# Kernel optimization log

Hardware: AMD Instinct MI355X
Metric: run time of the kernel (lower is better)

The kernel has to match this reference:

```python
import jax, jax.numpy as jnp
import numpy as np

N_CELL, N_WELL = 200000, 2000
E_CC, E_CW = 1200000, 200000
CF, WF, H = 16, 8, 128
NUM_PHASES, OUT_SEQ = 3, 25
OUT = NUM_PHASES * OUT_SEQ  # 75


def setup_inputs() -> dict:
    key = jax.random.key(0)
    ks = jax.random.split(key, 24)
    p = lambda k, shp: jax.random.normal(k, shp, dtype=jnp.float32) * 0.02
    return {
        "cell_x": jax.random.normal(ks[0], (N_CELL, CF), dtype=jnp.float32),
        "well_x": jax.random.normal(ks[1], (N_WELL, WF), dtype=jnp.float32),
        "edge_index_cell": jax.random.randint(ks[2], (2, E_CC), 0, N_CELL),
        "edge_well_src": jax.random.randint(ks[3], (E_CW,), 0, N_CELL),
        "edge_well_dst": jax.random.randint(ks[4], (E_CW,), 0, N_WELL),
        # input projections
        "W_cell": p(ks[5], (CF, H)), "b_cell": jnp.zeros((H,), jnp.float32),
        "W_well": p(ks[6], (WF, H)), "b_well": jnp.zeros((H,), jnp.float32),
        # SAGEConv cell->cell: lin_l (on aggregated neighbors, has bias), lin_r (on root, no bias)
        "Wl_cc": p(ks[7], (H, H)), "bl_cc": jnp.zeros((H,), jnp.float32),
        "Wr_cc": p(ks[8], (H, H)),
        # SAGEConv cell->well (bipartite)
        "Wl_cw": p(ks[9], (H, H)), "bl_cw": jnp.zeros((H,), jnp.float32),
        "Wr_cw": p(ks[10], (H, H)),
        # well MLP
        "W_m1": p(ks[11], (H, H)), "b_m1": jnp.zeros((H,), jnp.float32),
        "W_m2": p(ks[12], (H, OUT)), "b_m2": jnp.zeros((OUT,), jnp.float32),
    }


def _mean_aggr(msgs, dst, num_segments):
    # PyG 'mean' aggregation: sum per destination / neighbor count; 0 for isolated nodes.
    s = jax.ops.segment_sum(msgs, dst, num_segments=num_segments)
    c = jax.ops.segment_sum(jnp.ones((dst.shape[0], 1), msgs.dtype), dst, num_segments=num_segments)
    return s / jnp.maximum(c, 1.0)


def reference(cell_x, well_x, edge_index_cell, edge_well_src, edge_well_dst,
              W_cell, b_cell, W_well, b_well,
              Wl_cc, bl_cc, Wr_cc, Wl_cw, bl_cw, Wr_cw,
              W_m1, b_m1, W_m2, b_m2):
    cell_h = cell_x @ W_cell + b_cell                      # [N_cell, H]
    well_h = well_x @ W_well + b_well                      # [N_well, H]

    # SAGEConv(cell_h, edge_index_cell): gather source feats, mean-scatter to dst
    src, dst = edge_index_cell[0], edge_index_cell[1]
    agg_c = _mean_aggr(cell_h[src], dst, N_CELL)           # [N_cell, H]
    cell_h = agg_c @ Wl_cc + bl_cc + cell_h @ Wr_cc

    # Bipartite SAGEConv((cell_h, well_h), edge_well): aggregate cells into wells
    agg_w = _mean_aggr(cell_h[edge_well_src], edge_well_dst, N_WELL)  # [N_well, H]
    well_h = agg_w @ Wl_cw + bl_cw + well_h @ Wr_cw

    # well MLP head
    h = jax.nn.relu(well_h @ W_m1 + b_m1)
    out = h @ W_m2 + b_m2                                  # [N_well, 75]
    return out.reshape(-1, NUM_PHASES, OUT_SEQ)            # [N_well, 3, 25]
```

## Files before the change

kernel.cpp:

```cpp
#include <hip/hip_runtime.h>

#define N_CELL 200000
#define N_WELL 2000
#define E_CC   1200000
#define E_CW   200000
#define CF     16
#define WF     8
#define H      128
#define OUTF   75

#define CAP_C  16
#define CAP_W  224
#define OVF_CAP 16384
#define WPB    4

__device__ __forceinline__ float b2f(unsigned short u) {
    union { unsigned int i; float f; } v; v.i = ((unsigned int)u) << 16; return v.f;
}
__device__ __forceinline__ unsigned short f2b(float f) {
    union { float f; unsigned int i; } v; v.f = f;
    unsigned int i = v.i;
    return (unsigned short)((i + 0x7fffu + ((i >> 16) & 1u)) >> 16);
}
__device__ __forceinline__ float lo16(unsigned int v) { return b2f((unsigned short)(v & 0xffffu)); }
__device__ __forceinline__ float hi16(unsigned int v) { return b2f((unsigned short)(v >> 16)); }
__device__ __forceinline__ float ldf(const void* p, int i, int bf) {
    return bf ? b2f(((const unsigned short*)p)[i]) : ((const float*)p)[i];
}

__global__ __launch_bounds__(256) void k_sniff(const unsigned int* __restrict__ x, int* __restrict__ flag)
{
    __shared__ int cnt[256];
    int t = threadIdx.x;
    unsigned int d = x[t];
    unsigned int e = (d >> 7) & 0xffu;
    cnt[t] = (e >= 110u && e <= 135u) ? 1 : 0;
    __syncthreads();
    for (int o = 128; o > 0; o >>= 1) { if (t < o) cnt[t] += cnt[t + o]; __syncthreads(); }
    if (t == 0) flag[0] = (cnt[0] >= 192) ? 1 : 0;
}

__global__ __launch_bounds__(128) void k_precomp(const void* __restrict__ W_cell,
                                                 const void* __restrict__ b_cell,
                                                 const void* __restrict__ Wl,
                                                 const void* __restrict__ Wr,
                                                 const void* __restrict__ bl,
                                                 const int* __restrict__ flag,
                                                 float* __restrict__ G1, float* __restrict__ G2,
                                                 float* __restrict__ g1v, float* __restrict__ g2v)
{
    int f = threadIdx.x, b = blockIdx.x, bf = flag[0];
    if (b < 16) {
        float s1 = 0.f, s2 = 0.f;
        for (int j = 0; j < H; ++j) {
            float wc = ldf(W_cell, b * H + j, bf);
            s1 += wc * ldf(Wl, j * H + f, bf);
            s2 += wc * ldf(Wr, j * H + f, bf);
        }
        G1[b * H + f] = s1; G2[b * H + f] = s2;
    } else {
        float s1 = 0.f, s2 = 0.f;
        for (int j = 0; j < H; ++j) {
            float bc = ldf(b_cell, j, bf);
            s1 += bc * ldf(Wl, j * H + f, bf);
            s2 += bc * ldf(Wr, j * H + f, bf);
        }
        g1v[f] = s1; g2v[f] = s2 + ldf(bl, f, bf);
    }
}

__global__ __launch_bounds__(128) void k_precomp2(const float* __restrict__ G1, const float* __restrict__ G2,
                                                  const float* __restrict__ g1v, const float* __restrict__ g2v,
                                                  const void* __restrict__ Wl_cw,
                                                  const void* __restrict__ bl_cw,
                                                  const void* __restrict__ Wr_cw,
                                                  const void* __restrict__ W_well,
                                                  const void* __restrict__ b_well,
                                                  const int* __restrict__ flag,
                                                  float* __restrict__ A1, float* __restrict__ A2,
                                                  float* __restrict__ Bm,
                                                  float* __restrict__ a1, float* __restrict__ a2,
                                                  float* __restrict__ b0)
{
    int f = threadIdx.x, b = blockIdx.x, bf = flag[0];
    if (b < 16) {
        float s1 = 0.f, s2 = 0.f;
        for (int j = 0; j < H; ++j) {
            float wl = ldf(Wl_cw, j * H + f, bf);
            s1 += G1[b * H + j] * wl;
            s2 += G2[b * H + j] * wl;
        }
        A1[b * H + f] = s1; A2[b * H + f] = s2;
    } else if (b < 24) {
        int k = b - 16;
        float s = 0.f;
        for (int j = 0; j < H; ++j)
            s += ldf(W_well, k * H + j, bf) * ldf(Wr_cw, j * H + f, bf);
        Bm[k * H + f] = s;
    } else {
        float s1 = 0.f, s2 = 0.f, s3 = 0.f;
        for (int j = 0; j < H; ++j) {
            float wl = ldf(Wl_cw, j * H + f, bf);
            s1 += g1v[j] * wl;
            s2 += g2v[j] * wl;
            s3 += ldf(b_well, j, bf) * ldf(Wr_cw, j * H + f, bf);
        }
        a1[f] = s1; a2[f] = s2; b0[f] = s3 + ldf(bl_cw, f, bf);
    }
}

__global__ __launch_bounds__(256) void k_cvt(const void* __restrict__ Wm1, const void* __restrict__ Wm2,
                                             const void* __restrict__ bm1, const void* __restrict__ bm2,
                                             const int* __restrict__ flag,
                                             float* __restrict__ Wm1f, float* __restrict__ Wm2f,
                                             float* __restrict__ bm1f, float* __restrict__ bm2f)
{
    int i = blockIdx.x * 256 + threadIdx.x, bf = flag[0];
    if (i < H * H) Wm1f[i] = ldf(Wm1, i, bf);
    else if (i < H * H + H * OUTF) Wm2f[i - H * H] = ldf(Wm2, i - H * H, bf);
    else if (i < H * H + H * OUTF + H) bm1f[i - H * H - H * OUTF] = ldf(bm1, i - H * H - H * OUTF, bf);
    else if (i < H * H + H * OUTF + H + OUTF) bm2f[i - H * H - H * OUTF - H] = ldf(bm2, i - H * H - H * OUTF - H, bf);
}

__global__ void k_mark(const int* __restrict__ ews, unsigned char* __restrict__ mark)
{
    int i = blockIdx.x * 256 + threadIdx.x;
    if (i < E_CW) {
        unsigned c = (unsigned)ews[i];
        if (c < N_CELL) mark[c] = 1;
    }
}

__global__ void k_build(const int* __restrict__ cc_src, const int* __restrict__ cc_dst,
                        const int* __restrict__ ews, const int* __restrict__ ewd,
                        const unsigned char* __restrict__ mark,
                        int* __restrict__ counts_c, int* __restrict__ counts_w,
                        int* __restrict__ buckets_c, int* __restrict__ buckets_w,
                        int* __restrict__ ovf_cnt, int2* __restrict__ ovf)
{
    int i = blockIdx.x * 256 + threadIdx.x;
    if (i < E_CC) {
        unsigned d = (unsigned)cc_dst[i];
        if (d < N_CELL && mark[d]) {
            int s = atomicAdd(&counts_c[d], 1);
            if (s < CAP_C) buckets_c[d * CAP_C + s] = cc_src[i];
            else {
                int p = atomicAdd(ovf_cnt, 1);
                if (p < OVF_CAP) { ovf[p].x = (int)d; ovf[p].y = cc_src[i]; }
            }
        }
    } else if (i < E_CC + E_CW) {
        int j = i - E_CC;
        unsigned d = (unsigned)ewd[j];
        if (d < N_WELL) {
            int s = atomicAdd(&counts_w[d], 1);
            if (s < CAP_W) buckets_w[d * CAP_W + s] = ews[j];
        }
    }
}

__global__ __launch_bounds__(256) void k_aggA(const void* __restrict__ xr,
                                              const int* __restrict__ flag,
                                              const unsigned char* __restrict__ mark,
                                              const int* __restrict__ counts_c,
                                              const int* __restrict__ buckets_c,
                                              float* __restrict__ y)
{
    int gid = (blockIdx.x * 256 + threadIdx.x) >> 3;
    int jl = threadIdx.x & 7;
    if (gid >= N_CELL) return;
    if (!mark[gid]) return;
    int bf = flag[0];
    int cnt = counts_c[gid]; if (cnt < 0) cnt = 0;
    int lim = (cnt < CAP_C) ? cnt : CAP_C;
    float acc[16];
#pragma unroll
    for (int k = 0; k < 16; ++k) acc[k] = 0.f;

    for (int j = jl; j < lim; j += 8) {
        unsigned s = (unsigned)buckets_c[gid * CAP_C + j]; if (s >= N_CELL) s = 0;
        if (bf) {
            uint4 a = ((const uint4*)xr)[(size_t)s * 2];
            uint4 b = ((const uint4*)xr)[(size_t)s * 2 + 1];
            acc[0] += lo16(a.x);  acc[1] += hi16(a.x);
            acc[2] += lo16(a.y);  acc[3] += hi16(a.y);
            acc[4] += lo16(a.z);  acc[5] += hi16(a.z);
            acc[6] += lo16(a.w);  acc[7] += hi16(a.w);
            acc[8] += lo16(b.x);  acc[9] += hi16(b.x);
            acc[10] += lo16(b.y); acc[11] += hi16(b.y);
            acc[12] += lo16(b.z); acc[13] += hi16(b.z);
            acc[14] += lo16(b.w); acc[15] += hi16(b.w);
        } else {
            const float4* p = (const float4*)xr + (size_t)s * 4;
#pragma unroll
            for (int q = 0; q < 4; ++q) {
                float4 v = p[q];
                acc[4 * q]     += v.x; acc[4 * q + 1] += v.y;
                acc[4 * q + 2] += v.z; acc[4 * q + 3] += v.w;
            }
        }
    }
#pragma unroll
    for (int m = 1; m < 8; m <<= 1) {
#pragma unroll
        for (int k = 0; k < 16; ++k) acc[k] += __shfl_xor(acc[k], m, 64);
    }
    float sc = (cnt > 0) ? (1.0f / (float)cnt) : 0.0f;
    float2 st; st.x = acc[2 * jl] * sc; st.y = acc[2 * jl + 1] * sc;
    ((float2*)y)[(size_t)gid * 8 + jl] = st;
}

__global__ __launch_bounds__(256) void k_ovf(const void* __restrict__ xr,
                                             const int* __restrict__ flag,
                                             const int* __restrict__ ovf_cnt,
                                             const int2* __restrict__ ovf,
                                             const int* __restrict__ counts_c,
                                             float* __restrict__ y)
{
    int gid = (blockIdx.x * 256 + threadIdx.x) >> 3;
    int jl = threadIdx.x & 7;
    int n = ovf_cnt[0]; if (n > OVF_CAP) n = OVF_CAP;
    if (gid >= n) return;
    int bf = flag[0];
    unsigned d = (unsigned)ovf[gid].x; if (d >= N_CELL) d = 0;
    unsigned s = (unsigned)ovf[gid].y; if (s >= N_CELL) s = 0;
    int cnt = counts_c[d];
    float inv = (cnt > 0) ? (1.0f / (float)cnt) : 0.0f;
    float v0, v1;
    if (bf) {
        unsigned int u = ((const unsigned int*)xr)[(size_t)s * 8 + jl];
        v0 = lo16(u); v1 = hi16(u);
    } else {
        v0 = ((const float*)xr)[(size_t)s * 16 + 2 * jl];
        v1 = ((const float*)xr)[(size_t)s * 16 + 2 * jl + 1];
    }
    atomicAdd(&y[(size_t)d * 16 + 2 * jl], v0 * inv);
    atomicAdd(&y[(size_t)d * 16 + 2 * jl + 1], v1 * inv);
}

__global__ __launch_bounds__(256) void k_wellagg(const void* __restrict__ xr,
                                                 const int* __restrict__ flag,
                                                 const float* __restrict__ y,
                                                 const int* __restrict__ counts_c,
                                                 const int* __restrict__ counts_w,
                                                 const int* __restrict__ buckets_w,
                                                 const void* __restrict__ wx,
                                                 const float* __restrict__ A1, const float* __restrict__ A2,
                                                 const float* __restrict__ Bm,
                                                 const float* __restrict__ a1, const float* __restrict__ a2,
                                                 const float* __restrict__ b0,
                                                 float* __restrict__ Z)
{
    __shared__ float sP[16], sR[16], sq[1];
    int w = blockIdx.x, t = threadIdx.x, bf = flag[0];
    int g = t >> 3, jl = t & 7;
    if (t < 16) { sP[t] = 0.f; sR[t] = 0.f; }
    if (t == 16) sq[0] = 0.f;
    __syncthreads();

    int cntw = counts_w[w]; if (cntw < 0) cntw = 0;
    int lim = (cntw < CAP_W) ? cntw : CAP_W;

    float p0 = 0.f, p1 = 0.f, r0 = 0.f, r1 = 0.f, qn = 0.f;
    const unsigned int* x32 = (const unsigned int*)xr;
    const float* xf = (const float*)xr;

    for (int e = g; e < lim; e += 32) {
        unsigned c = (unsigned)buckets_w[w * CAP_W + e]; if (c >= N_CELL) c = 0;
        float2 yv = ((const float2*)y)[(size_t)c * 8 + jl];
        p0 += yv.x; p1 += yv.y;
        if (bf) {
            unsigned int u = x32[(size_t)c * 8 + jl];
            r0 += lo16(u); r1 += hi16(u);
        } else {
            r0 += xf[(size_t)c * 16 + 2 * jl];
            r1 += xf[(size_t)c * 16 + 2 * jl + 1];
        }
        if (jl == 0) qn += (counts_c[c] > 0) ? 1.0f : 0.0f;
    }
    atomicAdd(&sP[2 * jl], p0);
    atomicAdd(&sP[2 * jl + 1], p1);
    atomicAdd(&sR[2 * jl], r0);
    atomicAdd(&sR[2 * jl + 1], r1);
    if (jl == 0 && qn != 0.f) atomicAdd(&sq[0], qn);
    __syncthreads();

    int f = t;
    if (f < H) {
        float inv = (cntw > 0) ? (1.0f / (float)cntw) : 0.0f;
        float mask = (cntw > 0) ? 1.0f : 0.0f;
        float wh = (sq[0] * inv) * a1[f] + a2[f];
#pragma unroll
        for (int k = 0; k < 16; ++k)
            wh += (sP[k] * inv) * A1[k * H + f] + (sR[k] * inv) * A2[k * H + f];
        wh *= mask;
        wh += b0[f];
#pragma unroll
        for (int k = 0; k < WF; ++k)
            wh += ldf(wx, w * WF + k, bf) * Bm[k * H + f];
        Z[(size_t)w * H + f] = wh;
    }
}

__global__ __launch_bounds__(128) void k_head(const float* __restrict__ Z,
                                              const float* __restrict__ Wm1f, const float* __restrict__ Wm2f,
                                              const float* __restrict__ bm1f, const float* __restrict__ bm2f,
                                              const int* __restrict__ flag,
                                              void* __restrict__ outp)
{
    __shared__ float sz[WPB][H], sh[WPB][H];
    int w0 = blockIdx.x * WPB, t = threadIdx.x, bf = flag[0];
    float4 zv = ((const float4*)(Z + (size_t)w0 * H))[t];
    ((float4*)&sz[0][0])[t] = zv;
    __syncthreads();

    float acc[WPB];
#pragma unroll
    for (int i = 0; i < WPB; ++i) acc[i] = bm1f[t];
    for (int k = 0; k < H; ++k) {
        float wm = Wm1f[k * H + t];
#pragma unroll
        for (int i = 0; i < WPB; ++i) acc[i] += sz[i][k] * wm;
    }
#pragma unroll
    for (int i = 0; i < WPB; ++i) sh[i][t] = fmaxf(acc[i], 0.f);
    __syncthreads();

    if (t < OUTF) {
        float o[WPB];
#pragma unroll
        for (int i = 0; i < WPB; ++i) o[i] = bm2f[t];
        for (int k = 0; k < H; ++k) {
            float wm = Wm2f[k * OUTF + t];
#pragma unroll
            for (int i = 0; i < WPB; ++i) o[i] += sh[i][k] * wm;
        }
        if (bf) {
#pragma unroll
            for (int i = 0; i < WPB; ++i)
                ((unsigned short*)outp)[(size_t)(w0 + i) * OUTF + t] = f2b(o[i]);
        } else {
#pragma unroll
            for (int i = 0; i < WPB; ++i)
                ((float*)outp)[(size_t)(w0 + i) * OUTF + t] = o[i];
        }
    }
}

extern "C" void kernel_launch(void* const* d_in, const int* in_sizes, int n_in,
                              void* d_out, int out_size, void* d_ws, size_t ws_size,
                              hipStream_t stream)
{
    const void* cell_x = d_in[0];
    const void* well_x = d_in[1];
    const int* eic = (const int*)d_in[2];
    const int* ews = (const int*)d_in[3];
    const int* ewd = (const int*)d_in[4];
    const void* W_cell = d_in[5];
    const void* b_cell = d_in[6];
    const void* W_well = d_in[7];
    const void* b_well = d_in[8];
    const void* Wl_cc = d_in[9];
    const void* bl_cc = d_in[10];
    const void* Wr_cc = d_in[11];
    const void* Wl_cw = d_in[12];
    const void* bl_cw = d_in[13];
    const void* Wr_cw = d_in[14];
    const void* W_m1 = d_in[15];
    const void* b_m1 = d_in[16];
    const void* W_m2 = d_in[17];
    const void* b_m2 = d_in[18];
    (void)in_sizes; (void)n_in; (void)out_size; (void)ws_size;

    const int* cc_src = eic;
    const int* cc_dst = eic + E_CC;

    char* wsp = (char*)d_ws;
    size_t off = 0;
    auto carve = [&](size_t bytes) -> char* {
        char* p = wsp + off;
        off = (off + bytes + 255) & ~(size_t)255;
        return p;
    };

    float* G1   = (float*)carve(16 * H * 4);
    float* G2   = (float*)carve(16 * H * 4);
    float* g1v  = (float*)carve(H * 4);
    float* g2v  = (float*)carve(H * 4);
    float* A1   = (float*)carve(16 * H * 4);
    float* A2   = (float*)carve(16 * H * 4);
    float* Bm   = (float*)carve(WF * H * 4);
    float* a1   = (float*)carve(H * 4);
    float* a2   = (float*)carve(H * 4);
    float* b0   = (float*)carve(H * 4);
    float* Wm1f = (float*)carve(H * H * 4);
    float* Wm2f = (float*)carve(H * OUTF * 4);
    float* bm1f = (float*)carve(H * 4);
    float* bm2f = (float*)carve(OUTF * 4);
    int*   flag = (int*)carve(256);
    size_t zero_beg = off;
    int*   counts   = (int*)carve((size_t)(N_CELL + N_WELL) * 4);
    int*   counts_c = counts;
    int*   counts_w = counts + N_CELL;
    unsigned char* mark = (unsigned char*)carve((size_t)N_CELL);
    int*   ovf_cnt  = (int*)carve(256);
    size_t zero_end = off;
    int*   buckets_c = (int*)carve((size_t)N_CELL * CAP_C * 4);
    int*   buckets_w = (int*)carve((size_t)N_WELL * CAP_W * 4);
    float* y         = (float*)carve((size_t)N_CELL * 16 * 4);
    int2*  ovf       = (int2*)carve((size_t)OVF_CAP * 8);
    float* Z         = (float*)carve((size_t)N_WELL * H * 4);

    k_sniff<<<1, 256, 0, stream>>>((const unsigned int*)cell_x, flag);
    hipMemsetAsync((char*)d_ws + zero_beg, 0, zero_end - zero_beg, stream);
    k_precomp<<<17, 128, 0, stream>>>(W_cell, b_cell, Wl_cc, Wr_cc, bl_cc, flag, G1, G2, g1v, g2v);
    k_precomp2<<<25, 128, 0, stream>>>(G1, G2, g1v, g2v, Wl_cw, bl_cw, Wr_cw, W_well, b_well, flag,
                                       A1, A2, Bm, a1, a2, b0);
    k_cvt<<<(H * H + H * OUTF + H + OUTF + 255) / 256, 256, 0, stream>>>(W_m1, W_m2, b_m1, b_m2, flag,
                                                                         Wm1f, Wm2f, bm1f, bm2f);
    k_mark<<<(E_CW + 255) / 256, 256, 0, stream>>>(ews, mark);
    k_build<<<(E_CC + E_CW + 255) / 256, 256, 0, stream>>>(cc_src, cc_dst, ews, ewd, mark,
                                                           counts_c, counts_w, buckets_c, buckets_w,
                                                           ovf_cnt, ovf);
    k_aggA<<<(N_CELL * 8 + 255) / 256, 256, 0, stream>>>(cell_x, flag, mark, counts_c, buckets_c, y);
    k_ovf<<<(OVF_CAP * 8 + 255) / 256, 256, 0, stream>>>(cell_x, flag, ovf_cnt, ovf, counts_c, y);
    k_wellagg<<<N_WELL, 256, 0, stream>>>(cell_x, flag, y, counts_c, counts_w, buckets_w,
                                          well_x, A1, A2, Bm, a1, a2, b0, Z);
    k_head<<<N_WELL / WPB, 128, 0, stream>>>(Z, Wm1f, Wm2f, bm1f, bm2f, flag, d_out);
}
```

Baseline: 276.9 us.

## Replace per-cell edge buckets with bin-sorted edges and shared-memory aggregation

Cell-to-cell edges are no longer scattered into fixed-capacity per-destination buckets with an overflow path. They are now counting-sorted into 782 bins of 256 destination cells each, using a histogram, a scan and a scatter pass, and packed as source index plus local destination. Each bin is then aggregated in LDS with shared atomics, which also yields the neighbor counts. This removes the random global atomics on per-cell counters and the overflow kernel, but it reads the edge list twice and adds two kernel launches. The aggregation now relies on LDS float atomics.

```diff
diff --git a/kernel.cpp b/kernel.cpp
--- a/kernel.cpp
+++ b/kernel.cpp
@@ -9,10 +9,13 @@
 #define H      128
 #define OUTF   75
 
-#define CAP_C  16
 #define CAP_W  224
-#define OVF_CAP 16384
 #define WPB    4
+
+#define CPB    256
+#define NBIN   782
+#define NBLK_P 128
+#define CHUNK  9375
 
 __device__ __forceinline__ float b2f(unsigned short u) {
     union { unsigned int i; float f; } v; v.i = ((unsigned int)u) << 16; return v.f;
@@ -122,120 +125,147 @@
     else if (i < H * H + H * OUTF + H + OUTF) bm2f[i - H * H - H * OUTF - H] = ldf(bm2, i - H * H - H * OUTF - H, bf);
 }
 
-__global__ void k_mark(const int* __restrict__ ews, unsigned char* __restrict__ mark)
+__global__ void k_markw(const int* __restrict__ ews, const int* __restrict__ ewd,
+                        unsigned char* __restrict__ mark,
+                        int* __restrict__ counts_w, int* __restrict__ buckets_w)
 {
     int i = blockIdx.x * 256 + threadIdx.x;
     if (i < E_CW) {
         unsigned c = (unsigned)ews[i];
         if (c < N_CELL) mark[c] = 1;
-    }
-}
-
-__global__ void k_build(const int* __restrict__ cc_src, const int* __restrict__ cc_dst,
-                        const int* __restrict__ ews, const int* __restrict__ ewd,
-                        const unsigned char* __restrict__ mark,
-                        int* __restrict__ counts_c, int* __restrict__ counts_w,
-                        int* __restrict__ buckets_c, int* __restrict__ buckets_w,
-                        int* __restrict__ ovf_cnt, int2* __restrict__ ovf)
-{
-    int i = blockIdx.x * 256 + threadIdx.x;
-    if (i < E_CC) {
-        unsigned d = (unsigned)cc_dst[i];
-        if (d < N_CELL && mark[d]) {
-            int s = atomicAdd(&counts_c[d], 1);
-            if (s < CAP_C) buckets_c[d * CAP_C + s] = cc_src[i];
-            else {
-                int p = atomicAdd(ovf_cnt, 1);
-                if (p < OVF_CAP) { ovf[p].x = (int)d; ovf[p].y = cc_src[i]; }
-            }
-        }
-    } else if (i < E_CC + E_CW) {
-        int j = i - E_CC;
-        unsigned d = (unsigned)ewd[j];
+        unsigned d = (unsigned)ewd[i];
         if (d < N_WELL) {
             int s = atomicAdd(&counts_w[d], 1);
-            if (s < CAP_W) buckets_w[d * CAP_W + s] = ews[j];
-        }
-    }
-}
-
-__global__ __launch_bounds__(256) void k_aggA(const void* __restrict__ xr,
-                                              const int* __restrict__ flag,
+            if (s < CAP_W) buckets_w[d * CAP_W + s] = ews[i];
+        }
+    }
+}
+
+__global__ __launch_bounds__(256) void k_hist(const int* __restrict__ cc_dst,
                                               const unsigned char* __restrict__ mark,
-                                              const int* __restrict__ counts_c,
-                                              const int* __restrict__ buckets_c,
-                                              float* __restrict__ y)
-{
-    int gid = (blockIdx.x * 256 + threadIdx.x) >> 3;
-    int jl = threadIdx.x & 7;
-    if (gid >= N_CELL) return;
-    if (!mark[gid]) return;
-    int bf = flag[0];
-    int cnt = counts_c[gid]; if (cnt < 0) cnt = 0;
-    int lim = (cnt < CAP_C) ? cnt : CAP_C;
-    float acc[16];
-#pragma unroll
-    for (int k = 0; k < 16; ++k) acc[k] = 0.f;
-
-    for (int j = jl; j < lim; j += 8) {
-        unsigned s = (unsigned)buckets_c[gid * CAP_C + j]; if (s >= N_CELL) s = 0;
+                                              int* __restrict__ bin_cnt)
+{
+    __shared__ int hl[NBIN];
+    int t = threadIdx.x;
+    for (int i = t; i < NBIN; i += 256) hl[i] = 0;
+    __syncthreads();
+    int beg = blockIdx.x * CHUNK, end = beg + CHUNK; if (end > E_CC) end = E_CC;
+    for (int e = beg + t; e < end; e += 256) {
+        unsigned d = (unsigned)cc_dst[e];
+        if (d < N_CELL && mark[d]) atomicAdd(&hl[d >> 8], 1);
+    }
+    __syncthreads();
+    for (int i = t; i < NBIN; i += 256) if (hl[i]) atomicAdd(&bin_cnt[i], hl[i]);
+}
+
+__global__ __launch_bounds__(1024) void k_scanbins(const int* __restrict__ bin_cnt,
+                                                   int* __restrict__ bin_off, int* __restrict__ bin_cur)
+{
+    __shared__ int sm[1024];
+    int t = threadIdx.x;
+    sm[t] = (t < NBIN) ? bin_cnt[t] : 0;
+    __syncthreads();
+    for (int o = 1; o < 1024; o <<= 1) {
+        int u = (t >= o) ? sm[t - o] : 0;
+        __syncthreads();
+        sm[t] += u;
+        __syncthreads();
+    }
+    if (t < NBIN) {
+        int v = sm[t];
+        bin_off[t + 1] = v;
+        bin_cur[t] = v - bin_cnt[t];
+        if (t == 0) bin_off[0] = 0;
+    }
+}
+
+__global__ __launch_bounds__(256) void k_scatter(const int* __restrict__ cc_src,
+                                                 const int* __restrict__ cc_dst,
+                                                 const unsigned char* __restrict__ mark,
+                                                 int* __restrict__ bin_cur,
+                                                 unsigned int* __restrict__ binned)
+{
+    __shared__ int hl[NBIN];
+    __shared__ int cur[NBIN];
+    int t = threadIdx.x;
+    for (int i = t; i < NBIN; i += 256) hl[i] = 0;
+    __syncthreads();
+    int beg = blockIdx.x * CHUNK, end = beg + CHUNK; if (end > E_CC) end = E_CC;
+    for (int e = beg + t; e < end; e += 256) {
+        unsigned d = (unsigned)cc_dst[e];
+        if (d < N_CELL && mark[d]) atomicAdd(&hl[d >> 8], 1);
+    }
+    __syncthreads();
+    for (int i = t; i < NBIN; i += 256)
+        cur[i] = hl[i] ? atomicAdd(&bin_cur[i], hl[i]) : 0;
+    __syncthreads();
+    for (int e = beg + t; e < end; e += 256) {
+        unsigned d = (unsigned)cc_dst[e];
+        if (d < N_CELL && mark[d]) {
+            unsigned s = (unsigned)cc_src[e]; if (s >= N_CELL) s = 0;
+            int slot = atomicAdd(&cur[d >> 8], 1);
+            if ((unsigned)slot < E_CC)
+                binned[slot] = s | ((d & 255u) << 18);
+        }
+    }
+}
+
+__global__ __launch_bounds__(256) void k_binagg(const void* __restrict__ xr,
+                                                const int* __restrict__ flag,
+                                                const int* __restrict__ bin_off,
+                                                const unsigned int* __restrict__ binned,
+                                                float* __restrict__ y, int* __restrict__ counts_c)
+{
+    __shared__ float yl[CPB * 16];
+    __shared__ int   dl[CPB];
+    __shared__ float il[CPB];
+    int b = blockIdx.x, t = threadIdx.x, bf = flag[0];
+    for (int i = t; i < CPB * 16; i += 256) yl[i] = 0.f;
+    if (t < CPB) dl[t] = 0;
+    __syncthreads();
+    int beg = bin_off[b], end = bin_off[b + 1];
+    if (beg < 0) beg = 0;
+    if (end > E_CC) end = E_CC;
+    for (int e = beg + t; e < end; e += 256) {
+        unsigned p = binned[e];
+        unsigned s = p & 0x3FFFFu; if (s >= N_CELL) s = 0;
+        int dloc = (p >> 18) & 255;
+        atomicAdd(&dl[dloc], 1);
+        float* yr = &yl[dloc * 16];
         if (bf) {
             uint4 a = ((const uint4*)xr)[(size_t)s * 2];
-            uint4 b = ((const uint4*)xr)[(size_t)s * 2 + 1];
-            acc[0] += lo16(a.x);  acc[1] += hi16(a.x);
-            acc[2] += lo16(a.y);  acc[3] += hi16(a.y);
-            acc[4] += lo16(a.z);  acc[5] += hi16(a.z);
-            acc[6] += lo16(a.w);  acc[7] += hi16(a.w);
-            acc[8] += lo16(b.x);  acc[9] += hi16(b.x);
-            acc[10] += lo16(b.y); acc[11] += hi16(b.y);
-            acc[12] += lo16(b.z); acc[13] += hi16(b.z);
-            acc[14] += lo16(b.w); acc[15] += hi16(b.w);
+            uint4 bq = ((const uint4*)xr)[(size_t)s * 2 + 1];
+            atomicAdd(&yr[0],  lo16(a.x));  atomicAdd(&yr[1],  hi16(a.x));
+            atomicAdd(&yr[2],  lo16(a.y));  atomicAdd(&yr[3],  hi16(a.y));
+            atomicAdd(&yr[4],  lo16(a.z));  atomicAdd(&yr[5],  hi16(a.z));
+            atomicAdd(&yr[6],  lo16(a.w));  atomicAdd(&yr[7],  hi16(a.w));
+            atomicAdd(&yr[8],  lo16(bq.x)); atomicAdd(&yr[9],  hi16(bq.x));
+            atomicAdd(&yr[10], lo16(bq.y)); atomicAdd(&yr[11], hi16(bq.y));
+            atomicAdd(&yr[12], lo16(bq.z)); atomicAdd(&yr[13], hi16(bq.z));
+            atomicAdd(&yr[14], lo16(bq.w)); atomicAdd(&yr[15], hi16(bq.w));
         } else {
-            const float4* p = (const float4*)xr + (size_t)s * 4;
+            const float4* pp = (const float4*)xr + (size_t)s * 4;
 #pragma unroll
             for (int q = 0; q < 4; ++q) {
-                float4 v = p[q];
-                acc[4 * q]     += v.x; acc[4 * q + 1] += v.y;
-                acc[4 * q + 2] += v.z; acc[4 * q + 3] += v.w;
+                float4 v = pp[q];
+                atomicAdd(&yr[4 * q],     v.x); atomicAdd(&yr[4 * q + 1], v.y);
+                atomicAdd(&yr[4 * q + 2], v.z); atomicAdd(&yr[4 * q + 3], v.w);
             }
         }
     }
-#pragma unroll
-    for (int m = 1; m < 8; m <<= 1) {
-#pragma unroll
-        for (int k = 0; k < 16; ++k) acc[k] += __shfl_xor(acc[k], m, 64);
-    }
-    float sc = (cnt > 0) ? (1.0f / (float)cnt) : 0.0f;
-    float2 st; st.x = acc[2 * jl] * sc; st.y = acc[2 * jl + 1] * sc;
-    ((float2*)y)[(size_t)gid * 8 + jl] = st;
-}
-
-__global__ __launch_bounds__(256) void k_ovf(const void* __restrict__ xr,
-                                             const int* __restrict__ flag,
-                                             const int* __restrict__ ovf_cnt,
-                                             const int2* __restrict__ ovf,
-                                             const int* __restrict__ counts_c,
-                                             float* __restrict__ y)
-{
-    int gid = (blockIdx.x * 256 + threadIdx.x) >> 3;
-    int jl = threadIdx.x & 7;
-    int n = ovf_cnt[0]; if (n > OVF_CAP) n = OVF_CAP;
-    if (gid >= n) return;
-    int bf = flag[0];
-    unsigned d = (unsigned)ovf[gid].x; if (d >= N_CELL) d = 0;
-    unsigned s = (unsigned)ovf[gid].y; if (s >= N_CELL) s = 0;
-    int cnt = counts_c[d];
-    float inv = (cnt > 0) ? (1.0f / (float)cnt) : 0.0f;
-    float v0, v1;
-    if (bf) {
-        unsigned int u = ((const unsigned int*)xr)[(size_t)s * 8 + jl];
-        v0 = lo16(u); v1 = hi16(u);
-    } else {
-        v0 = ((const float*)xr)[(size_t)s * 16 + 2 * jl];
-        v1 = ((const float*)xr)[(size_t)s * 16 + 2 * jl + 1];
-    }
-    atomicAdd(&y[(size_t)d * 16 + 2 * jl], v0 * inv);
-    atomicAdd(&y[(size_t)d * 16 + 2 * jl + 1], v1 * inv);
+    __syncthreads();
+    if (t < CPB) {
+        int d = dl[t];
+        il[t] = (d > 0) ? (1.0f / (float)d) : 0.f;
+        int c = b * CPB + t;
+        if (c < N_CELL) counts_c[c] = d;
+    }
+    __syncthreads();
+    size_t base = (size_t)b * CPB * 16;
+    for (int i = t; i < CPB * 16; i += 256) {
+        int cl = i >> 4;
+        if (b * CPB + cl < N_CELL) y[base + i] = yl[i] * il[cl];
+    }
 }
 
 __global__ __launch_bounds__(256) void k_wellagg(const void* __restrict__ xr,
@@ -403,12 +433,13 @@
     int*   counts_c = counts;
     int*   counts_w = counts + N_CELL;
     unsigned char* mark = (unsigned char*)carve((size_t)N_CELL);
-    int*   ovf_cnt  = (int*)carve(256);
+    int*   bin_cnt = (int*)carve((size_t)(NBIN + 2) * 4);
     size_t zero_end = off;
-    int*   buckets_c = (int*)carve((size_t)N_CELL * CAP_C * 4);
+    int*   bin_off  = (int*)carve((size_t)(NBIN + 2) * 4);
+    int*   bin_cur  = (int*)carve((size_t)(NBIN + 2) * 4);
+    unsigned int* binned = (unsigned int*)carve((size_t)E_CC * 4);
     int*   buckets_w = (int*)carve((size_t)N_WELL * CAP_W * 4);
-    float* y         = (float*)carve((size_t)N_CELL * 16 * 4);
-    int2*  ovf       = (int2*)carve((size_t)OVF_CAP * 8);
+    float* y         = (float*)carve((size_t)NBIN * CPB * 16 * 4);
     float* Z         = (float*)carve((size_t)N_WELL * H * 4);
 
     k_sniff<<<1, 256, 0, stream>>>((const unsigned int*)cell_x, flag);
@@ -418,12 +449,11 @@
                                        A1, A2, Bm, a1, a2, b0);
     k_cvt<<<(H * H + H * OUTF + H + OUTF + 255) / 256, 256, 0, stream>>>(W_m1, W_m2, b_m1, b_m2, flag,
                                                                          Wm1f, Wm2f, bm1f, bm2f);
-    k_mark<<<(E_CW + 255) / 256, 256, 0, stream>>>(ews, mark);
-    k_build<<<(E_CC + E_CW + 255) / 256, 256, 0, stream>>>(cc_src, cc_dst, ews, ewd, mark,
-                                                           counts_c, counts_w, buckets_c, buckets_w,
-                                                           ovf_cnt, ovf);
-    k_aggA<<<(N_CELL * 8 + 255) / 256, 256, 0, stream>>>(cell_x, flag, mark, counts_c, buckets_c, y);
-    k_ovf<<<(OVF_CAP * 8 + 255) / 256, 256, 0, stream>>>(cell_x, flag, ovf_cnt, ovf, counts_c, y);
+    k_markw<<<(E_CW + 255) / 256, 256, 0, stream>>>(ews, ewd, mark, counts_w, buckets_w);
+    k_hist<<<NBLK_P, 256, 0, stream>>>(cc_dst, mark, bin_cnt);
+    k_scanbins<<<1, 1024, 0, stream>>>(bin_cnt, bin_off, bin_cur);
+    k_scatter<<<NBLK_P, 256, 0, stream>>>(cc_src, cc_dst, mark, bin_cur, binned);
+    k_binagg<<<NBIN, 256, 0, stream>>>(cell_x, flag, bin_off, binned, y, counts_c);
     k_wellagg<<<N_WELL, 256, 0, stream>>>(cell_x, flag, y, counts_c, counts_w, buckets_w,
                                           well_x, A1, A2, Bm, a1, a2, b0, Z);
     k_head<<<N_WELL / WPB, 128, 0, stream>>>(Z, Wm1f, Wm2f, bm1f, bm2f, flag, d_out);
```

Measured after the change: 367.6 us. 1.33x slower.

## Fold weight conversion into precompute, merge well bucketing with marking, batch edge loads

Applied to the files above, without the earlier changes.

Merges the k_cvt weight conversion into k_precomp2 through extra blocks and fuses well-edge bucketing into the marking kernel, which removes two launches. k_build now handles four cell edges per thread with all loads issued before the atomics, giving more memory-level parallelism. k_aggA replaces its neighbor loop with two unrolled gathers issued up front. The risk is lower occupancy from the larger per-thread work and register pressure; CAP_C=16 still bounds the two gathers per lane.

```diff
diff --git a/kernel.cpp b/kernel.cpp
--- a/kernel.cpp
+++ b/kernel.cpp
@@ -14,6 +14,9 @@
 #define OVF_CAP 16384
 #define WPB    4
 
+#define BLD_T  307200
+#define MKW_T  50176
+
 __device__ __forceinline__ float b2f(unsigned short u) {
     union { unsigned int i; float f; } v; v.i = ((unsigned int)u) << 16; return v.f;
 }
@@ -76,11 +79,15 @@
                                                   const void* __restrict__ Wr_cw,
                                                   const void* __restrict__ W_well,
                                                   const void* __restrict__ b_well,
+                                                  const void* __restrict__ Wm1, const void* __restrict__ Wm2,
+                                                  const void* __restrict__ bm1, const void* __restrict__ bm2,
                                                   const int* __restrict__ flag,
                                                   float* __restrict__ A1, float* __restrict__ A2,
                                                   float* __restrict__ Bm,
                                                   float* __restrict__ a1, float* __restrict__ a2,
-                                                  float* __restrict__ b0)
+                                                  float* __restrict__ b0,
+                                                  float* __restrict__ Wm1f, float* __restrict__ Wm2f,
+                                                  float* __restrict__ bm1f, float* __restrict__ bm2f)
 {
     int f = threadIdx.x, b = blockIdx.x, bf = flag[0];
     if (b < 16) {
@@ -97,7 +104,7 @@
         for (int j = 0; j < H; ++j)
             s += ldf(W_well, k * H + j, bf) * ldf(Wr_cw, j * H + f, bf);
         Bm[k * H + f] = s;
-    } else {
+    } else if (b == 24) {
         float s1 = 0.f, s2 = 0.f, s3 = 0.f;
         for (int j = 0; j < H; ++j) {
             float wl = ldf(Wl_cw, j * H + f, bf);
@@ -106,56 +113,74 @@
             s3 += ldf(b_well, j, bf) * ldf(Wr_cw, j * H + f, bf);
         }
         a1[f] = s1; a2[f] = s2; b0[f] = s3 + ldf(bl_cw, f, bf);
-    }
-}
-
-__global__ __launch_bounds__(256) void k_cvt(const void* __restrict__ Wm1, const void* __restrict__ Wm2,
-                                             const void* __restrict__ bm1, const void* __restrict__ bm2,
-                                             const int* __restrict__ flag,
-                                             float* __restrict__ Wm1f, float* __restrict__ Wm2f,
-                                             float* __restrict__ bm1f, float* __restrict__ bm2f)
-{
-    int i = blockIdx.x * 256 + threadIdx.x, bf = flag[0];
-    if (i < H * H) Wm1f[i] = ldf(Wm1, i, bf);
-    else if (i < H * H + H * OUTF) Wm2f[i - H * H] = ldf(Wm2, i - H * H, bf);
-    else if (i < H * H + H * OUTF + H) bm1f[i - H * H - H * OUTF] = ldf(bm1, i - H * H - H * OUTF, bf);
-    else if (i < H * H + H * OUTF + H + OUTF) bm2f[i - H * H - H * OUTF - H] = ldf(bm2, i - H * H - H * OUTF - H, bf);
-}
-
-__global__ void k_mark(const int* __restrict__ ews, unsigned char* __restrict__ mark)
+    } else {
+        int i = (b - 25) * 128 + f;
+        if (i < H * H) Wm1f[i] = ldf(Wm1, i, bf);
+        else if (i < H * H + H * OUTF) Wm2f[i - H * H] = ldf(Wm2, i - H * H, bf);
+        else if (i < H * H + H * OUTF + H) bm1f[i - H * H - H * OUTF] = ldf(bm1, i - H * H - H * OUTF, bf);
+        else if (i < H * H + H * OUTF + H + OUTF) bm2f[i - H * H - H * OUTF - H] = ldf(bm2, i - H * H - H * OUTF - H, bf);
+    }
+}
+
+__global__ __launch_bounds__(256) void k_markw(const int* __restrict__ ews, const int* __restrict__ ewd,
+                                               unsigned char* __restrict__ mark,
+                                               int* __restrict__ counts_w, int* __restrict__ buckets_w)
 {
     int i = blockIdx.x * 256 + threadIdx.x;
-    if (i < E_CW) {
-        unsigned c = (unsigned)ews[i];
-        if (c < N_CELL) mark[c] = 1;
-    }
-}
-
-__global__ void k_build(const int* __restrict__ cc_src, const int* __restrict__ cc_dst,
-                        const int* __restrict__ ews, const int* __restrict__ ewd,
-                        const unsigned char* __restrict__ mark,
-                        int* __restrict__ counts_c, int* __restrict__ counts_w,
-                        int* __restrict__ buckets_c, int* __restrict__ buckets_w,
-                        int* __restrict__ ovf_cnt, int2* __restrict__ ovf)
+#pragma unroll
+    for (int u = 0; u < 4; ++u) {
+        int e = i + u * MKW_T;
+        if (e < E_CW) {
+            unsigned c = (unsigned)ews[e];
+            if (c < N_CELL) mark[c] = 1;
+            unsigned d = (unsigned)ewd[e];
+            if (d < N_WELL) {
+                int s = atomicAdd(&counts_w[d], 1);
+                if (s < CAP_W) buckets_w[d * CAP_W + s] = (int)c;
+            }
+        }
+    }
+}
+
+__global__ __launch_bounds__(256) void k_build(const int* __restrict__ cc_src, const int* __restrict__ cc_dst,
+                                               const unsigned char* __restrict__ mark,
+                                               int* __restrict__ counts_c,
+                                               int* __restrict__ buckets_c,
+                                               int* __restrict__ ovf_cnt, int2* __restrict__ ovf)
 {
     int i = blockIdx.x * 256 + threadIdx.x;
-    if (i < E_CC) {
-        unsigned d = (unsigned)cc_dst[i];
-        if (d < N_CELL && mark[d]) {
-            int s = atomicAdd(&counts_c[d], 1);
-            if (s < CAP_C) buckets_c[d * CAP_C + s] = cc_src[i];
-            else {
-                int p = atomicAdd(ovf_cnt, 1);
-                if (p < OVF_CAP) { ovf[p].x = (int)d; ovf[p].y = cc_src[i]; }
-            }
-        }
-    } else if (i < E_CC + E_CW) {
-        int j = i - E_CC;
-        unsigned d = (unsigned)ewd[j];
-        if (d < N_WELL) {
-            int s = atomicAdd(&counts_w[d], 1);
-            if (s < CAP_W) buckets_w[d * CAP_W + s] = ews[j];
-        }
+    int e0 = i, e1 = i + BLD_T, e2 = i + 2 * BLD_T, e3 = i + 3 * BLD_T;
+    unsigned d0 = (e0 < E_CC) ? (unsigned)cc_dst[e0] : 0xFFFFFFFFu;
+    unsigned d1 = (e1 < E_CC) ? (unsigned)cc_dst[e1] : 0xFFFFFFFFu;
+    unsigned d2 = (e2 < E_CC) ? (unsigned)cc_dst[e2] : 0xFFFFFFFFu;
+    unsigned d3 = (e3 < E_CC) ? (unsigned)cc_dst[e3] : 0xFFFFFFFFu;
+    bool m0 = (d0 < N_CELL) && mark[d0];
+    bool m1 = (d1 < N_CELL) && mark[d1];
+    bool m2 = (d2 < N_CELL) && mark[d2];
+    bool m3 = (d3 < N_CELL) && mark[d3];
+    int s0 = m0 ? cc_src[e0] : 0;
+    int s1 = m1 ? cc_src[e1] : 0;
+    int s2 = m2 ? cc_src[e2] : 0;
+    int s3 = m3 ? cc_src[e3] : 0;
+    if (m0) {
+        int p = atomicAdd(&counts_c[d0], 1);
+        if (p < CAP_C) buckets_c[d0 * CAP_C + p] = s0;
+        else { int q = atomicAdd(ovf_cnt, 1); if (q < OVF_CAP) { ovf[q].x = (int)d0; ovf[q].y = s0; } }
+    }
+    if (m1) {
+        int p = atomicAdd(&counts_c[d1], 1);
+        if (p < CAP_C) buckets_c[d1 * CAP_C + p] = s1;
+        else { int q = atomicAdd(ovf_cnt, 1); if (q < OVF_CAP) { ovf[q].x = (int)d1; ovf[q].y = s1; } }
+    }
+    if (m2) {
+        int p = atomicAdd(&counts_c[d2], 1);
+        if (p < CAP_C) buckets_c[d2 * CAP_C + p] = s2;
+        else { int q = atomicAdd(ovf_cnt, 1); if (q < OVF_CAP) { ovf[q].x = (int)d2; ovf[q].y = s2; } }
+    }
+    if (m3) {
+        int p = atomicAdd(&counts_c[d3], 1);
+        if (p < CAP_C) buckets_c[d3 * CAP_C + p] = s3;
+        else { int q = atomicAdd(ovf_cnt, 1); if (q < OVF_CAP) { ovf[q].x = (int)d3; ovf[q].y = s3; } }
     }
 }
 
@@ -177,26 +202,52 @@
 #pragma unroll
     for (int k = 0; k < 16; ++k) acc[k] = 0.f;
 
-    for (int j = jl; j < lim; j += 8) {
-        unsigned s = (unsigned)buckets_c[gid * CAP_C + j]; if (s >= N_CELL) s = 0;
-        if (bf) {
-            uint4 a = ((const uint4*)xr)[(size_t)s * 2];
-            uint4 b = ((const uint4*)xr)[(size_t)s * 2 + 1];
-            acc[0] += lo16(a.x);  acc[1] += hi16(a.x);
-            acc[2] += lo16(a.y);  acc[3] += hi16(a.y);
-            acc[4] += lo16(a.z);  acc[5] += hi16(a.z);
-            acc[6] += lo16(a.w);  acc[7] += hi16(a.w);
-            acc[8] += lo16(b.x);  acc[9] += hi16(b.x);
-            acc[10] += lo16(b.y); acc[11] += hi16(b.y);
-            acc[12] += lo16(b.z); acc[13] += hi16(b.z);
-            acc[14] += lo16(b.w); acc[15] += hi16(b.w);
-        } else {
-            const float4* p = (const float4*)xr + (size_t)s * 4;
+    int j0 = jl, j1 = jl + 8;
+    unsigned s0 = (j0 < lim) ? (unsigned)buckets_c[gid * CAP_C + j0] : 0xFFFFFFFFu;
+    unsigned s1 = (j1 < lim) ? (unsigned)buckets_c[gid * CAP_C + j1] : 0xFFFFFFFFu;
+    if (s0 >= N_CELL) s0 = 0xFFFFFFFFu;
+    if (s1 >= N_CELL) s1 = 0xFFFFFFFFu;
+
+    if (bf) {
+        uint4 a0, b0q, a1, b1q;
+        bool v0 = (s0 != 0xFFFFFFFFu), v1 = (s1 != 0xFFFFFFFFu);
+        if (v0) { a0 = ((const uint4*)xr)[(size_t)s0 * 2]; b0q = ((const uint4*)xr)[(size_t)s0 * 2 + 1]; }
+        if (v1) { a1 = ((const uint4*)xr)[(size_t)s1 * 2]; b1q = ((const uint4*)xr)[(size_t)s1 * 2 + 1]; }
+        if (v0) {
+            acc[0] += lo16(a0.x);  acc[1] += hi16(a0.x);
+            acc[2] += lo16(a0.y);  acc[3] += hi16(a0.y);
+            acc[4] += lo16(a0.z);  acc[5] += hi16(a0.z);
+            acc[6] += lo16(a0.w);  acc[7] += hi16(a0.w);
+            acc[8] += lo16(b0q.x); acc[9] += hi16(b0q.x);
+            acc[10] += lo16(b0q.y); acc[11] += hi16(b0q.y);
+            acc[12] += lo16(b0q.z); acc[13] += hi16(b0q.z);
+            acc[14] += lo16(b0q.w); acc[15] += hi16(b0q.w);
+        }
+        if (v1) {
+            acc[0] += lo16(a1.x);  acc[1] += hi16(a1.x);
+            acc[2] += lo16(a1.y);  acc[3] += hi16(a1.y);
+            acc[4] += lo16(a1.z);  acc[5] += hi16(a1.z);
+            acc[6] += lo16(a1.w);  acc[7] += hi16(a1.w);
+            acc[8] += lo16(b1q.x); acc[9] += hi16(b1q.x);
+            acc[10] += lo16(b1q.y); acc[11] += hi16(b1q.y);
+            acc[12] += lo16(b1q.z); acc[13] += hi16(b1q.z);
+            acc[14] += lo16(b1q.w); acc[15] += hi16(b1q.w);
+        }
+    } else {
+        if (s0 != 0xFFFFFFFFu) {
+            const float4* p = (const float4*)xr + (size_t)s0 * 4;
 #pragma unroll
             for (int q = 0; q < 4; ++q) {
                 float4 v = p[q];
-                acc[4 * q]     += v.x; acc[4 * q + 1] += v.y;
-                acc[4 * q + 2] += v.z; acc[4 * q + 3] += v.w;
+                acc[4 * q] += v.x; acc[4 * q + 1] += v.y; acc[4 * q + 2] += v.z; acc[4 * q + 3] += v.w;
+            }
+        }
+        if (s1 != 0xFFFFFFFFu) {
+            const float4* p = (const float4*)xr + (size_t)s1 * 4;
+#pragma unroll
+            for (int q = 0; q < 4; ++q) {
+                float4 v = p[q];
+                acc[4 * q] += v.x; acc[4 * q + 1] += v.y; acc[4 * q + 2] += v.z; acc[4 * q + 3] += v.w;
             }
         }
     }
@@ -414,14 +465,11 @@
     k_sniff<<<1, 256, 0, stream>>>((const unsigned int*)cell_x, flag);
     hipMemsetAsync((char*)d_ws + zero_beg, 0, zero_end - zero_beg, stream);
     k_precomp<<<17, 128, 0, stream>>>(W_cell, b_cell, Wl_cc, Wr_cc, bl_cc, flag, G1, G2, g1v, g2v);
-    k_precomp2<<<25, 128, 0, stream>>>(G1, G2, g1v, g2v, Wl_cw, bl_cw, Wr_cw, W_well, b_well, flag,
-                                       A1, A2, Bm, a1, a2, b0);
-    k_cvt<<<(H * H + H * OUTF + H + OUTF + 255) / 256, 256, 0, stream>>>(W_m1, W_m2, b_m1, b_m2, flag,
-                                                                         Wm1f, Wm2f, bm1f, bm2f);
-    k_mark<<<(E_CW + 255) / 256, 256, 0, stream>>>(ews, mark);
-    k_build<<<(E_CC + E_CW + 255) / 256, 256, 0, stream>>>(cc_src, cc_dst, ews, ewd, mark,
-                                                           counts_c, counts_w, buckets_c, buckets_w,
-                                                           ovf_cnt, ovf);
+    k_precomp2<<<230, 128, 0, stream>>>(G1, G2, g1v, g2v, Wl_cw, bl_cw, Wr_cw, W_well, b_well,
+                                        W_m1, W_m2, b_m1, b_m2, flag,
+                                        A1, A2, Bm, a1, a2, b0, Wm1f, Wm2f, bm1f, bm2f);
+    k_markw<<<MKW_T / 256, 256, 0, stream>>>(ews, ewd, mark, counts_w, buckets_w);
+    k_build<<<BLD_T / 256, 256, 0, stream>>>(cc_src, cc_dst, mark, counts_c, buckets_c, ovf_cnt, ovf);
     k_aggA<<<(N_CELL * 8 + 255) / 256, 256, 0, stream>>>(cell_x, flag, mark, counts_c, buckets_c, y);
     k_ovf<<<(OVF_CAP * 8 + 255) / 256, 256, 0, stream>>>(cell_x, flag, ovf_cnt, ovf, counts_c, y);
     k_wellagg<<<N_WELL, 256, 0, stream>>>(cell_x, flag, y, counts_c, counts_w, buckets_w,
```

New measurement: 295.4 us. +6.7%, slower.
